# Optimization experiments

Measured on AMD Instinct MI355X. Metric: run time of the kernel, lower is better.

The kernel has to match this reference:

```python
import jax, jax.numpy as jnp
import numpy as np

B, N, E, F, C = 4, 10000, 160000, 128, 128
NUM_ITERATIONS = 3  # num_iterations init arg


def setup_inputs() -> dict:
    key = jax.random.key(0)
    ks = jax.random.split(key, 8)
    objects = jax.random.normal(ks[0], (B, N, F), dtype=jnp.float32)
    connections = jax.random.randint(ks[1], (B, E, 2), 0, N, dtype=jnp.int32)
    # small init scales keep exp() in the attention numerically tame (mirrors
    # glorot/orthogonal-scale weights at init)
    object_state_W = jax.random.normal(ks[2], (F, C), dtype=jnp.float32) * (1.0 / np.sqrt(F))
    state_attention_W = jax.random.normal(ks[3], (C, C), dtype=jnp.float32) * 0.05
    linked_state_attention_W = jax.random.normal(ks[4], (C, C), dtype=jnp.float32) * 0.05
    linked_state_W = jax.random.normal(ks[5], (C, C), dtype=jnp.float32) * (1.0 / np.sqrt(C))
    attention_b = jnp.zeros((C,), dtype=jnp.float32)
    state_b = jnp.zeros((C,), dtype=jnp.float32)
    return {
        "objects": objects,
        "object_state_W": object_state_W,
        "state_attention_W": state_attention_W,
        "linked_state_attention_W": linked_state_attention_W,
        "attention_b": attention_b,
        "linked_state_W": linked_state_W,
        "state_b": state_b,
        "connections": connections,
    }


def reference(objects, object_state_W, state_attention_W, linked_state_attention_W,
              attention_b, linked_state_W, state_b, connections):
    # bidirectional: double edges with both orientations  [B, 2E]
    src = jnp.concatenate([connections[:, :, 0], connections[:, :, 1]], axis=1)
    dst = jnp.concatenate([connections[:, :, 1], connections[:, :, 0]], axis=1)

    # initial states: [B, N, C]
    states = jnp.tanh(jnp.einsum('bnf,fc->bnc', objects, object_state_W) + state_b)

    def step_one(states_b, src_b, dst_b):
        # states_b: [N, C]; src_b/dst_b: [2E]
        states_aW = states_b @ state_attention_W          # [N, C]
        linked_aW = states_b @ linked_state_attention_W   # [N, C]
        # per-edge unnormalized attention  [2E, C]
        attention = jnp.exp(states_aW[src_b] + linked_aW[dst_b] + attention_b)
        # scatter-add normalization; self edge contributes 1 (exp(0))
        attention_norm = jnp.ones_like(states_b).at[src_b].add(attention)  # [N, C]
        self_attention = 1.0 / attention_norm
        attention = attention / attention_norm[src_b]
        # weighted neighbor aggregation
        attented = attention * states_b[dst_b]                              # [2E, C]
        linked_gated = jnp.zeros_like(states_b).at[src_b].add(attented)     # [N, C]
        return jnp.tanh(states_b * self_attention + linked_gated @ linked_state_W + state_b)

    step = jax.vmap(step_one)
    for _ in range(NUM_ITERATIONS):
        states = step(states, src, dst)
    return states
```

## Files before the change

kernel.cpp:

```cpp
#include <hip/hip_runtime.h>
#include <hip/hip_bf16.h>


#define BATCH 4
#define NNODE 10000
#define NEDGE 160000
#define TWOE  (2*NEDGE)
#define MROWS (BATCH*NNODE)
#define NCHUNK 64
#define CHUNKE (NEDGE/NCHUNK)
#define PADN  10240

typedef unsigned short u16;
typedef unsigned int   u32;
typedef __attribute__((ext_vector_type(8))) short bf16x8_t;
typedef __attribute__((ext_vector_type(4))) float f32x4_t;

__device__ __forceinline__ float b2f(u16 h){ return __uint_as_float(((u32)h) << 16); }
__device__ __forceinline__ u16 f2bf(float f){
  u32 u = __float_as_uint(f);
  return (u16)((u + 0x7fffu + ((u >> 16) & 1u)) >> 16);
}
__device__ __forceinline__ float fast_tanh(float x){
  float e = __expf(2.0f * x);
  return fmaf(-2.0f, __builtin_amdgcn_rcpf(e + 1.0f), 1.0f);
}

__global__ void detect_dtype(const u32* __restrict__ objw, int* __restrict__ flag){
  __shared__ int zc, hc;
  if (threadIdx.x == 0){ zc = 0; hc = 0; }
  __syncthreads();
  int z = 0, h = 0;
  for (int i = threadIdx.x; i < 1024; i += 256){
    u32 lo = objw[i] & 0xffffu;
    if (lo == 0) z++;
    if (((lo >> 7) & 0xffu) >= 160u) h++;
  }
  atomicAdd(&zc, z); atomicAdd(&hc, h);
  __syncthreads();
  if (threadIdx.x == 0) *flag = (hc > 0 || zc > 512) ? 1 : 0;
}

__global__ void prep_weights(const void* __restrict__ Wo, const void* __restrict__ Wa,
                             const void* __restrict__ Wla, const void* __restrict__ Wl,
                             const void* __restrict__ ab, const void* __restrict__ sb,
                             const int* __restrict__ flag, u16* __restrict__ Wt,
                             float* __restrict__ biasf){
  int idx = blockIdx.x * 256 + threadIdx.x;
  bool f = (*flag != 0);
  if (idx < 65536){
    int m = idx >> 14, k = (idx >> 7) & 127, c = idx & 127;
    const void* src = (m == 0) ? Wo : (m == 1) ? Wa : (m == 2) ? Wla : Wl;
    u16 h = f ? f2bf(((const float*)src)[k * 128 + c]) : ((const u16*)src)[k * 128 + c];
    Wt[m * 16384 + c * 128 + k] = h;
  } else {
    int t = idx - 65536;
    const void* src = (t < 128) ? sb : ab;
    int i = t & 127;
    biasf[t] = f ? ((const float*)src)[i] : b2f(((const u16*)src)[i]);
  }
}

__device__ __forceinline__ void chunk_of(int blk, int& b, int& c){
  int xcd = blk & 7;
  b = xcd >> 1;
  c = ((blk >> 3) << 1) | (xcd & 1);
}

__global__ void __launch_bounds__(256) csr_hist(const int* __restrict__ conn,
                                                u16* __restrict__ partial){
  int b, c; chunk_of(blockIdx.x, b, c);
  __shared__ u32 hist[NNODE];
  for (int n = threadIdx.x; n < NNODE; n += 256) hist[n] = 0;
  __syncthreads();
  const int2* cp = (const int2*)conn + (size_t)b * NEDGE + c * CHUNKE;
  for (int i = threadIdx.x; i < CHUNKE; i += 256){
    int2 e = cp[i];
    atomicAdd(&hist[e.x], 1);
    atomicAdd(&hist[e.y], 1);
  }
  __syncthreads();
  u16* prow = partial + (size_t)(b * NCHUNK + c) * PADN;
  for (int n = threadIdx.x; n < NNODE; n += 256) prow[n] = (u16)hist[n];
}

__global__ void __launch_bounds__(256) csr_colscan(u16* __restrict__ partial,
    int* __restrict__ row_start, int* __restrict__ bsum){
  int b = blockIdx.x / 40, w = blockIdx.x % 40;
  int n = w * 256 + threadIdx.x;
  u32 run = 0;
  if (n < NNODE){
    #pragma unroll 8
    for (int c = 0; c < NCHUNK; c++){
      size_t idx = (size_t)(b * NCHUNK + c) * PADN + n;
      u32 v = partial[idx];
      partial[idx] = (u16)run;
      run += v;
    }
  }
  __shared__ u32 buf[256];
  buf[threadIdx.x] = run;
  __syncthreads();
  for (int off = 1; off < 256; off <<= 1){
    u32 x = (threadIdx.x >= (unsigned)off) ? buf[threadIdx.x - off] : 0;
    __syncthreads();
    buf[threadIdx.x] += x;
    __syncthreads();
  }
  u32 incl = buf[threadIdx.x];
  if (n < NNODE) row_start[b * (NNODE + 1) + n] = (int)(incl - run);
  if (threadIdx.x == 255) bsum[blockIdx.x] = (int)incl;
}

__global__ void scanB(const int* __restrict__ bsum, int* __restrict__ boff,
                      int* __restrict__ row_start){
  __shared__ int s[160];
  if (threadIdx.x < 160) s[threadIdx.x] = bsum[threadIdx.x];
  __syncthreads();
  if (threadIdx.x < 160){
    int b = threadIdx.x / 40, j = threadIdx.x % 40;
    int off = 0;
    for (int q = b * 40; q < b * 40 + j; q++) off += s[q];
    boff[threadIdx.x] = off;
  }
  if (threadIdx.x < BATCH) row_start[threadIdx.x * (NNODE + 1) + NNODE] = TWOE;
}

__global__ void scanC(int* __restrict__ row_start, const int* __restrict__ boff){
  int b = blockIdx.x / 40, j = blockIdx.x % 40;
  int n = j * 256 + threadIdx.x;
  if (n < NNODE) row_start[b * (NNODE + 1) + n] += boff[blockIdx.x];
}

__global__ void __launch_bounds__(256) csr_fill(const int* __restrict__ conn,
    const u16* __restrict__ partial, const int* __restrict__ row_start,
    int* __restrict__ edge_dst){
  int b, c; chunk_of(blockIdx.x, b, c);
  __shared__ u32 cur[NNODE];
  const u16* prow = partial + (size_t)(b * NCHUNK + c) * PADN;
  const int* rs = row_start + b * (NNODE + 1);
  for (int n = threadIdx.x; n < NNODE; n += 256) cur[n] = (u32)rs[n] + prow[n];
  __syncthreads();
  const int2* cp = (const int2*)conn + (size_t)b * NEDGE + c * CHUNKE;
  int* edb = edge_dst + (size_t)b * TWOE;
  for (int i = threadIdx.x; i < CHUNKE; i += 256){
    int2 e = cp[i];
    u32 p1 = atomicAdd(&cur[e.x], 1); edb[p1] = e.y;
    u32 p2 = atomicAdd(&cur[e.y], 1); edb[p2] = e.x;
  }
}

__device__ __forceinline__ void gemm_tile4(const u16* __restrict__ arow,
    const u16* __restrict__ wt, int lm, int lq, int cofs, f32x4_t acc[4]){
  #pragma unroll
  for (int ks = 0; ks < 4; ks++){
    bf16x8_t a = *(const bf16x8_t*)(arow + ks * 32);
    #pragma unroll
    for (int nb = 0; nb < 4; nb++){
      bf16x8_t bfr = *(const bf16x8_t*)(wt + (cofs + nb * 16 + lm) * 128 + ks * 32 + lq * 8);
      acc[nb] = __builtin_amdgcn_mfma_f32_16x16x32_bf16(a, bfr, acc[nb], 0, 0, 0);
    }
  }
}

__device__ __forceinline__ void gemm_tile4_packed(const u32* __restrict__ Lrow,
    const u16* __restrict__ wt, int lm, int lq, int cofs, f32x4_t acc[4]){
  #pragma unroll
  for (int ks = 0; ks < 4; ks++){
    uint4 wa = *(const uint4*)(Lrow + ks * 32 + lq * 8);
    uint4 wb = *(const uint4*)(Lrow + ks * 32 + lq * 8 + 4);
    bf16x8_t a;
    a[0] = (short)wa.x; a[1] = (short)wa.y; a[2] = (short)wa.z; a[3] = (short)wa.w;
    a[4] = (short)wb.x; a[5] = (short)wb.y; a[6] = (short)wb.z; a[7] = (short)wb.w;
    #pragma unroll
    for (int nb = 0; nb < 4; nb++){
      bf16x8_t bfr = *(const bf16x8_t*)(wt + (cofs + nb * 16 + lm) * 128 + ks * 32 + lq * 8);
      acc[nb] = __builtin_amdgcn_mfma_f32_16x16x32_bf16(a, bfr, acc[nb], 0, 0, 0);
    }
  }
}

__device__ __forceinline__ void phase2_awlaw4(const u16* __restrict__ ldstile,
    const u16* __restrict__ Wt, const float* __restrict__ biasf,
    int lm, int lq, int cofs, int r0, _Float16* __restrict__ eat,
    u32* __restrict__ ghw){
  const u16* Wta  = Wt + 16384;
  const u16* Wtla = Wt + 32768;
  const u16* ldsrow = ldstile + lm * 136 + lq * 8;
  f32x4_t accA[4], accL[4];
  #pragma unroll
  for (int i = 0; i < 4; i++){ accA[i] = (f32x4_t){0.f,0.f,0.f,0.f}; accL[i] = (f32x4_t){0.f,0.f,0.f,0.f}; }
  #pragma unroll
  for (int ks = 0; ks < 4; ks++){
    bf16x8_t a = *(const bf16x8_t*)(ldsrow + ks * 32);
    #pragma unroll
    for (int nb = 0; nb < 4; nb++){
      bf16x8_t ba = *(const bf16x8_t*)(Wta  + (cofs + nb * 16 + lm) * 128 + ks * 32 + lq * 8);
      bf16x8_t bl = *(const bf16x8_t*)(Wtla + (cofs + nb * 16 + lm) * 128 + ks * 32 + lq * 8);
      accA[nb] = __builtin_amdgcn_mfma_f32_16x16x32_bf16(a, ba, accA[nb], 0, 0, 0);
      accL[nb] = __builtin_amdgcn_mfma_f32_16x16x32_bf16(a, bl, accL[nb], 0, 0, 0);
    }
  }
  #pragma unroll
  for (int nb = 0; nb < 4; nb++){
    int col = cofs + nb * 16 + lm;
    float bb = biasf[128 + col];
    #pragma unroll
    for (int i = 0; i < 4; i++){
      int row = r0 + lq * 4 + i;
      float ea = fminf(__expf(accA[nb][i]), 60000.0f);
      eat[(lq * 4 + i) * 128 + col] = (_Float16)ea;
      _Float16 elh = (_Float16)fminf(__expf(accL[nb][i] + bb), 60000.0f);
      u16 sbf = ldstile[(lq * 4 + i) * 136 + col];
      _Float16 sh = (_Float16)b2f(sbf);
      u32 elu = (u32)(*(const u16*)&elh);
      u32 shu = (u32)(*(const u16*)&sh);
      ghw[(size_t)row * 64 + (col & 63)] = elu | (shu << 16);
    }
  }
}

__device__ __forceinline__ void eah_writeback(const _Float16* __restrict__ eat,
    _Float16* __restrict__ eah, int blk_r0, int tid){
  const uint4* src = (const uint4*)eat;
  uint4* dst = (uint4*)(eah + (size_t)blk_r0 * 128);
  dst[tid]       = src[tid];
  dst[tid + 256] = src[tid + 256];
}

__global__ void __launch_bounds__(256) fused_init(const void* __restrict__ obj_raw,
    const int* __restrict__ flag, const u16* __restrict__ Wt,
    const float* __restrict__ biasf, _Float16* __restrict__ eah,
    u32* __restrict__ gat0, u32* __restrict__ gat1){
  __shared__ u16 lds[2][16 * 136];
  __shared__ _Float16 eat[2][16 * 128];
  const int lane = threadIdx.x & 63, wave = threadIdx.x >> 6;
  const int t = wave >> 1, ch = wave & 1, cofs = ch * 64;
  const int r0 = blockIdx.x * 32 + t * 16;
  const int lm = lane & 15, lq = lane >> 4;
  f32x4_t acc[4];
  #pragma unroll
  for (int i = 0; i < 4; i++) acc[i] = (f32x4_t){0.f, 0.f, 0.f, 0.f};
  if (*flag){
    const float* arow = (const float*)obj_raw + (size_t)(r0 + lm) * 128 + lq * 8;
    #pragma unroll
    for (int ks = 0; ks < 4; ks++){
      float4 fa = *(const float4*)(arow + ks * 32);
      float4 fb = *(const float4*)(arow + ks * 32 + 4);
      bf16x8_t a;
      a[0] = (short)f2bf(fa.x); a[1] = (short)f2bf(fa.y);
      a[2] = (short)f2bf(fa.z); a[3] = (short)f2bf(fa.w);
      a[4] = (short)f2bf(fb.x); a[5] = (short)f2bf(fb.y);
      a[6] = (short)f2bf(fb.z); a[7] = (short)f2bf(fb.w);
      #pragma unroll
      for (int nb = 0; nb < 4; nb++){
        bf16x8_t bfr = *(const bf16x8_t*)(Wt + (cofs + nb * 16 + lm) * 128 + ks * 32 + lq * 8);
        acc[nb] = __builtin_amdgcn_mfma_f32_16x16x32_bf16(a, bfr, acc[nb], 0, 0, 0);
      }
    }
  } else {
    gemm_tile4((const u16*)obj_raw + (size_t)(r0 + lm) * 128 + lq * 8, Wt, lm, lq, cofs, acc);
  }
  #pragma unroll
  for (int nb = 0; nb < 4; nb++){
    int col = cofs + nb * 16 + lm;
    float bb = biasf[col];
    #pragma unroll
    for (int i = 0; i < 4; i++)
      lds[t][(lq * 4 + i) * 136 + col] = f2bf(fast_tanh(acc[nb][i] + bb));
  }
  __syncthreads();
  phase2_awlaw4(&lds[t][0], Wt, biasf, lm, lq, cofs, r0, &eat[t][0], ch ? gat1 : gat0);
  __syncthreads();
  eah_writeback(&eat[0][0], eah, blockIdx.x * 32, threadIdx.x);
}

__global__ void __launch_bounds__(256) fused_mid(const u32* __restrict__ lgsa,
    const u16* __restrict__ Wt, const float* __restrict__ biasf,
    _Float16* __restrict__ eah, u32* __restrict__ gat0, u32* __restrict__ gat1){
  __shared__ u16 lds[2][16 * 136];
  __shared__ _Float16 eat[2][16 * 128];
  const int lane = threadIdx.x & 63, wave = threadIdx.x >> 6;
  const int t = wave >> 1, ch = wave & 1, cofs = ch * 64;
  const int r0 = blockIdx.x * 32 + t * 16;
  const int lm = lane & 15, lq = lane >> 4;
  f32x4_t acc[4];
  #pragma unroll
  for (int i = 0; i < 4; i++) acc[i] = (f32x4_t){0.f, 0.f, 0.f, 0.f};
  gemm_tile4_packed(lgsa + (size_t)(r0 + lm) * 128, Wt + 49152, lm, lq, cofs, acc);
  #pragma unroll
  for (int nb = 0; nb < 4; nb++){
    int col = cofs + nb * 16 + lm;
    float bb = biasf[col];
    #pragma unroll
    for (int i = 0; i < 4; i++){
      int row = r0 + lq * 4 + i;
      u32 v = lgsa[(size_t)row * 128 + col];
      u16 hb = (u16)(v >> 16);
      float sa = (float)(*(const _Float16*)&hb);
      lds[t][(lq * 4 + i) * 136 + col] = f2bf(fast_tanh(sa + acc[nb][i] + bb));
    }
  }
  __syncthreads();
  phase2_awlaw4(&lds[t][0], Wt, biasf, lm, lq, cofs, r0, &eat[t][0], ch ? gat1 : gat0);
  __syncthreads();
  eah_writeback(&eat[0][0], eah, blockIdx.x * 32, threadIdx.x);
}

__global__ void __launch_bounds__(256) final_out(const u32* __restrict__ lgsa,
    const u16* __restrict__ Wt, const float* __restrict__ biasf,
    const int* __restrict__ flag, void* __restrict__ outp){
  const int lane = threadIdx.x & 63, wave = threadIdx.x >> 6;
  const int t = wave >> 1, ch = wave & 1, cofs = ch * 64;
  const int r0 = blockIdx.x * 32 + t * 16;
  const int lm = lane & 15, lq = lane >> 4;
  bool f32out = (*flag != 0);
  f32x4_t acc[4];
  #pragma unroll
  for (int i = 0; i < 4; i++) acc[i] = (f32x4_t){0.f, 0.f, 0.f, 0.f};
  gemm_tile4_packed(lgsa + (size_t)(r0 + lm) * 128, Wt + 49152, lm, lq, cofs, acc);
  #pragma unroll
  for (int nb = 0; nb < 4; nb++){
    int col = cofs + nb * 16 + lm;
    float bb = biasf[col];
    #pragma unroll
    for (int i = 0; i < 4; i++){
      int row = r0 + lq * 4 + i;
      u32 vv = lgsa[(size_t)row * 128 + col];
      u16 hb = (u16)(vv >> 16);
      float sa = (float)(*(const _Float16*)&hb);
      float v = fast_tanh(sa + acc[nb][i] + bb);
      if (f32out) ((float*)outp)[(size_t)row * 128 + col] = v;
      else        ((u16*)  outp)[(size_t)row * 128 + col] = f2bf(v);
    }
  }
}

__device__ __forceinline__ void acc2(u32 g, float& a1, float& a2){
  union { u32 u; _Float16 h[2]; } cv; cv.u = g;
  float el = (float)cv.h[0];
  float sv = (float)cv.h[1];
  a1 += el;
  a2 = fmaf(el, sv, a2);
}

__global__ void __launch_bounds__(256) edge_kernel(const _Float16* __restrict__ eah,
    const u32* __restrict__ gat0, const u32* __restrict__ gat1,
    const int* __restrict__ row_start, const int* __restrict__ edge_dst,
    u32* __restrict__ lgsa){
  int blk = blockIdx.x;
  int xcd = blk & 7;
  int b = xcd >> 1, h = xcd & 1;
  int i = blk >> 3;
  int n = i * 4 + (int)(threadIdx.x >> 6);
  int node = b * NNODE + n;
  int c = threadIdx.x & 63;
  const u32* gh = (h ? gat1 : gat0) + (size_t)b * NNODE * 64;
  const u32* ghc = gh + c;
  int e0 = __builtin_amdgcn_readfirstlane(row_start[b * (NNODE + 1) + n]);
  int e1 = __builtin_amdgcn_readfirstlane(row_start[b * (NNODE + 1) + n + 1]);
  const int* ed = edge_dst + (size_t)b * TWOE;

  float ea = (float)eah[(size_t)node * 128 + h * 64 + c];
  u32 self = ghc[(size_t)n << 6];

  float s1 = 0.f, s2 = 0.f, t1 = 0.f, t2 = 0.f;
  int len = e1 - e0;
  int e = e0;
  for (int gi = len >> 4; gi > 0; gi--, e += 16){
    int d[16]; u32 g[16];
    #pragma unroll
    for (int j = 0; j < 16; j++) d[j] = ed[e + j];
    #pragma unroll
    for (int j = 0; j < 16; j++) g[j] = ghc[(size_t)d[j] << 6];
    #pragma unroll
    for (int j = 0; j < 16; j++) acc2(g[j], (j & 1) ? t1 : s1, (j & 1) ? t2 : s2);
  }
  if (len & 15){
    #pragma unroll
    for (int j = 0; j < 16; j++){
      int idx = e + j;
      int idc = idx < e1 ? idx : e1 - 1;
      u32 gg = ghc[(size_t)ed[idc] << 6];
      gg &= (u32)((idx - e1) >> 31);
      acc2(gg, (j & 1) ? t1 : s1, (j & 1) ? t2 : s2);
    }
  }
  s1 += t1; s2 += t2;
  float inv = __builtin_amdgcn_rcpf(fmaf(ea, s1, 1.0f));
  float lg = ea * s2 * inv;
  u16 hb = (u16)(self >> 16);
  float s_self = (float)(*(const _Float16*)&hb);
  _Float16 hs = (_Float16)(s_self * inv);
  u32 pk = (u32)f2bf(lg) | ((u32)(*(const u16*)&hs) << 16);
  lgsa[(size_t)node * 128 + h * 64 + c] = pk;
}

extern "C" void kernel_launch(void* const* d_in, const int* in_sizes, int n_in,
                              void* d_out, int out_size, void* d_ws, size_t ws_size,
                              hipStream_t stream){
  (void)in_sizes; (void)n_in; (void)ws_size; (void)out_size;
  const void* objects = d_in[0];
  const void* Wo      = d_in[1];
  const void* Wa      = d_in[2];
  const void* Wla     = d_in[3];
  const void* attn_b  = d_in[4];
  const void* Wl      = d_in[5];
  const void* state_b = d_in[6];
  const int*  conn    = (const int*)d_in[7];

  char* base = (char*)d_ws;
  size_t off = 0;
  auto alloc = [&](size_t bytes) -> char* {
    char* p = base + off;
    off = (off + bytes + 255) & ~(size_t)255;
    return p;
  };
  int*      flag      = (int*)     alloc(256);
  u16*      Wt        = (u16*)     alloc((size_t)4 * 16384 * 2);
  float*    biasf     = (float*)   alloc(256 * 4);
  _Float16* eah       = (_Float16*)alloc((size_t)MROWS * 128 * 2);
  u32*      gat0      = (u32*)     alloc((size_t)MROWS * 64 * 4);
  u32*      gat1      = (u32*)     alloc((size_t)MROWS * 64 * 4);
  u32*      lgsa      = (u32*)     alloc((size_t)MROWS * 128 * 4);
  u16*      partial   = (u16*)     alloc((size_t)BATCH * NCHUNK * PADN * 2);
  int*      row_start = (int*)     alloc((size_t)BATCH * (NNODE + 1) * 4);
  int*      edge_dst  = (int*)     alloc((size_t)BATCH * TWOE * 4);
  int*      bsum      = (int*)     alloc(160 * 4);
  int*      boff      = (int*)     alloc(160 * 4);

  detect_dtype<<<1, 256, 0, stream>>>((const u32*)objects, flag);
  prep_weights<<<257, 256, 0, stream>>>(Wo, Wa, Wla, Wl, attn_b, state_b, flag, Wt, biasf);

  csr_hist<<<256, 256, 0, stream>>>(conn, partial);
  csr_colscan<<<160, 256, 0, stream>>>(partial, row_start, bsum);
  scanB<<<1, 256, 0, stream>>>(bsum, boff, row_start);
  scanC<<<160, 256, 0, stream>>>(row_start, boff);
  csr_fill<<<256, 256, 0, stream>>>(conn, partial, row_start, edge_dst);

  fused_init<<<MROWS / 32, 256, 0, stream>>>(objects, flag, Wt, biasf, eah, gat0, gat1);
  edge_kernel<<<MROWS / 2, 256, 0, stream>>>(eah, gat0, gat1, row_start, edge_dst, lgsa);
  fused_mid<<<MROWS / 32, 256, 0, stream>>>(lgsa, Wt, biasf, eah, gat0, gat1);
  edge_kernel<<<MROWS / 2, 256, 0, stream>>>(eah, gat0, gat1, row_start, edge_dst, lgsa);
  fused_mid<<<MROWS / 32, 256, 0, stream>>>(lgsa, Wt, biasf, eah, gat0, gat1);
  edge_kernel<<<MROWS / 2, 256, 0, stream>>>(eah, gat0, gat1, row_start, edge_dst, lgsa);
  final_out<<<MROWS / 32, 256, 0, stream>>>(lgsa, Wt, biasf, flag, d_out);
}
```

Baseline: 399.7 us.

## Software-pipeline edge index loads and use fma_mix for fp16 accumulation

The edge gather loop now processes edges in groups of 8 and prefetches the next group's destination indices while the current group's gathered values are loaded and accumulated. The fp16-to-fp32 conversion plus add/fma is replaced with inline v_fma_mix_f32 instructions that read the packed halves directly. The masked 16-wide tail becomes a scalar remainder loop. The aim is to hide the dependent index-load latency and cut VALU conversion work, at the cost of fewer loads in flight per group and a serial tail.

New measurement: 375.6 us. -6.0%, faster.

```diff
diff --git a/kernel.cpp b/kernel.cpp
--- a/kernel.cpp
+++ b/kernel.cpp
@@ -336,12 +336,11 @@
   }
 }
 
-__device__ __forceinline__ void acc2(u32 g, float& a1, float& a2){
-  union { u32 u; _Float16 h[2]; } cv; cv.u = g;
-  float el = (float)cv.h[0];
-  float sv = (float)cv.h[1];
-  a1 += el;
-  a2 = fmaf(el, sv, a2);
+__device__ __forceinline__ void acc_mix(u32 g, float one, float& a1, float& a2){
+  asm("v_fma_mix_f32 %0, %2, %3, %0 op_sel:[0,0,0] op_sel_hi:[1,0,0]\n\t"
+      "v_fma_mix_f32 %1, %2, %2, %1 op_sel:[0,1,0] op_sel_hi:[1,1,0]"
+      : "+v"(a1), "+v"(a2)
+      : "v"(g), "v"(one));
 }
 
 __global__ void __launch_bounds__(256) edge_kernel(const _Float16* __restrict__ eah,
@@ -363,28 +362,34 @@
 
   float ea = (float)eah[(size_t)node * 128 + h * 64 + c];
   u32 self = ghc[(size_t)n << 6];
+  const float one = 1.0f;
 
   float s1 = 0.f, s2 = 0.f, t1 = 0.f, t2 = 0.f;
   int len = e1 - e0;
   int e = e0;
-  for (int gi = len >> 4; gi > 0; gi--, e += 16){
-    int d[16]; u32 g[16];
-    #pragma unroll
-    for (int j = 0; j < 16; j++) d[j] = ed[e + j];
-    #pragma unroll
-    for (int j = 0; j < 16; j++) g[j] = ghc[(size_t)d[j] << 6];
-    #pragma unroll
-    for (int j = 0; j < 16; j++) acc2(g[j], (j & 1) ? t1 : s1, (j & 1) ? t2 : s2);
-  }
-  if (len & 15){
-    #pragma unroll
-    for (int j = 0; j < 16; j++){
-      int idx = e + j;
-      int idc = idx < e1 ? idx : e1 - 1;
-      u32 gg = ghc[(size_t)ed[idc] << 6];
-      gg &= (u32)((idx - e1) >> 31);
-      acc2(gg, (j & 1) ? t1 : s1, (j & 1) ? t2 : s2);
-    }
+  int rem = len >> 3;
+  int d[8];
+  if (rem){
+    #pragma unroll
+    for (int j = 0; j < 8; j++) d[j] = ed[e0 + j];
+  }
+  for (; rem > 0; rem--){
+    u32 g[8];
+    #pragma unroll
+    for (int j = 0; j < 8; j++) g[j] = ghc[(size_t)d[j] << 6];
+    int ep = e + (rem > 1 ? 8 : 0);
+    int dn[8];
+    #pragma unroll
+    for (int j = 0; j < 8; j++) dn[j] = ed[ep + j];
+    #pragma unroll
+    for (int j = 0; j < 8; j++) acc_mix(g[j], one, (j & 1) ? t1 : s1, (j & 1) ? t2 : s2);
+    #pragma unroll
+    for (int j = 0; j < 8; j++) d[j] = dn[j];
+    e += 8;
+  }
+  for (; e < e1; e++){
+    u32 gg = ghc[(size_t)ed[e] << 6];
+    acc_mix(gg, one, s1, s2);
   }
   s1 += t1; s2 += t2;
   float inv = __builtin_amdgcn_rcpf(fmaf(ea, s1, 1.0f));
```
